# Kernel optimization log

Hardware: AMD Instinct MI355X
Metric: run time of the kernel (lower is better)

## Reference

```python
import jax, jax.numpy as jnp
import numpy as np

# static multi-scale pyramid (must match spatial_shapes array in setup_inputs)
SPATIAL = ((100, 100), (50, 50), (25, 25), (13, 13))
E, H, L, P = 256, 8, 4, 8   # embed_dims, num_heads, num_levels, num_points
BS, NQ = 2, 10000
LEN_VAL = sum(h * w for h, w in SPATIAL)


def _bilinear_gather(val, grid, Hs, Ws):
    """val: [BH, Hs*Ws, d]; grid: [BH, N, 2] in [-1,1].
    Matches F.grid_sample(mode='bilinear', padding_mode='zeros', align_corners=False)."""
    x = (grid[..., 0] + 1.0) * (Ws * 0.5) - 0.5
    y = (grid[..., 1] + 1.0) * (Hs * 0.5) - 0.5
    x0 = jnp.floor(x).astype(jnp.int32)
    y0 = jnp.floor(y).astype(jnp.int32)
    x1, y1 = x0 + 1, y0 + 1
    wx1 = x - x0.astype(x.dtype)
    wy1 = y - y0.astype(y.dtype)
    wx0, wy0 = 1.0 - wx1, 1.0 - wy1

    def corner(xi, yi, w):
        valid = (xi >= 0) & (xi < Ws) & (yi >= 0) & (yi < Hs)
        idx = jnp.clip(yi, 0, Hs - 1) * Ws + jnp.clip(xi, 0, Ws - 1)  # [BH, N]
        v = jnp.take_along_axis(val, idx[..., None], axis=1)          # [BH, N, d]
        return v * (w * valid.astype(w.dtype))[..., None]

    return (corner(x0, y0, wx0 * wy0) + corner(x1, y0, wx1 * wy0)
            + corner(x0, y1, wx0 * wy1) + corner(x1, y1, wx1 * wy1))


def setup_inputs() -> dict:
    key = jax.random.key(0)
    ks = jax.random.split(key, 10)
    scale = 1.0 / np.sqrt(E)
    inp = {
        'query': jax.random.normal(ks[0], (BS, NQ, E), jnp.float32),
        'value': jax.random.normal(ks[1], (BS, LEN_VAL, E), jnp.float32),
        'query_pos': 0.1 * jax.random.normal(ks[2], (BS, NQ, E), jnp.float32),
        'reference_points': jax.random.uniform(ks[3], (BS, NQ, L, 2), jnp.float32),
        'spatial_shapes': jnp.array(SPATIAL, dtype=jnp.int32),
        'W_off': 0.02 * jax.random.normal(ks[4], (E, H * L * P * 2), jnp.float32),
        'b_off': 0.5 * jax.random.normal(ks[5], (H * L * P * 2,), jnp.float32),
        'W_attn': 0.02 * jax.random.normal(ks[6], (E, H * L * P), jnp.float32),
        'b_attn': jnp.zeros((H * L * P,), jnp.float32),
        'W_val': scale * jax.random.normal(ks[7], (E, E), jnp.float32),
        'b_val': jnp.zeros((E,), jnp.float32),
        'W_out': scale * jax.random.normal(ks[8], (E, E), jnp.float32),
        'b_out': jnp.zeros((E,), jnp.float32),
    }
    return inp


def reference(query, value, query_pos, reference_points, spatial_shapes,
              W_off, b_off, W_attn, b_attn, W_val, b_val, W_out, b_out):
    d = E // H
    q = query + query_pos                                        # [bs, nq, E]
    bs, nq, _ = q.shape
    v = (value @ W_val + b_val).reshape(bs, LEN_VAL, H, d)       # [bs, len, H, d]
    off = (q @ W_off + b_off).reshape(bs, nq, H, L, P, 2)
    aw = jax.nn.softmax((q @ W_attn + b_attn).reshape(bs, nq, H, L * P), axis=-1)
    aw = aw.reshape(bs, nq, H, L, P)
    # normalizer is (W, H) per level
    norm = jnp.stack([spatial_shapes[:, 1], spatial_shapes[:, 0]], -1).astype(q.dtype)
    loc = reference_points[:, :, None, :, None, :] + off / norm[None, None, None, :, None, :]
    grids = 2.0 * loc - 1.0                                      # [bs, nq, H, L, P, 2]

    out = jnp.zeros((bs, nq, H, d), q.dtype)
    start = 0
    for lvl, (Hs, Ws) in enumerate(SPATIAL):
        v_l = v[:, start:start + Hs * Ws]                        # [bs, HW, H, d]
        start += Hs * Ws
        v_l = v_l.transpose(0, 2, 1, 3).reshape(bs * H, Hs * Ws, d)
        g_l = grids[:, :, :, lvl].transpose(0, 2, 1, 3, 4).reshape(bs * H, nq * P, 2)
        s = _bilinear_gather(v_l, g_l, Hs, Ws).reshape(bs, H, nq, P, d)
        w_l = aw[:, :, :, lvl].transpose(0, 2, 1, 3)             # [bs, H, nq, P]
        out = out + jnp.einsum('bhnpc,bhnp->bnhc', s, w_l)
    return out.reshape(bs, nq, E) @ W_out + b_out
```

## Files before the change

kernel.cpp:

```cpp
#include <hip/hip_runtime.h>


#define EE   256
#define HH   8
#define LL   4
#define NQq  10000
#define BSB  2
#define LENV 13294
#define MQ   16
#define ROWS_V (BSB * LENV)

#define VWS_OFF 393216

typedef unsigned short u16;
typedef unsigned int   u32;
typedef __attribute__((ext_vector_type(8))) short bf16x8;
typedef __attribute__((ext_vector_type(4))) float f32x4;

__device__ __forceinline__ u32 bf16_of(float f) {
  u32 u = __float_as_uint(f);
  return (u + 0x7FFFu + ((u >> 16) & 1u)) >> 16;
}
__device__ __forceinline__ float blo(u32 u) { return __uint_as_float(u << 16); }
__device__ __forceinline__ float bhi(u32 u) { return __uint_as_float(u & 0xFFFF0000u); }

__device__ __forceinline__ uint4 pack8(const float* f) {
  uint4 u;
  u.x = bf16_of(f[0]) | (bf16_of(f[1]) << 16);
  u.y = bf16_of(f[2]) | (bf16_of(f[3]) << 16);
  u.z = bf16_of(f[4]) | (bf16_of(f[5]) << 16);
  u.w = bf16_of(f[6]) | (bf16_of(f[7]) << 16);
  return u;
}

__device__ __forceinline__ void acc8(float o[8], uint4 q, float w) {
  o[0] += w * blo(q.x); o[1] += w * bhi(q.x);
  o[2] += w * blo(q.y); o[3] += w * bhi(q.y);
  o[4] += w * blo(q.z); o[5] += w * bhi(q.z);
  o[6] += w * blo(q.w); o[7] += w * bhi(q.w);
}

__global__ __launch_bounds__(64) void k_prep(
    const float* __restrict__ W_off, const float* __restrict__ W_attn,
    const float* __restrict__ W_val, const float* __restrict__ W_out,
    u16* __restrict__ wcat, u16* __restrict__ wval, u16* __restrict__ wout) {
  const int tile = blockIdx.x >> 3, s = blockIdx.x & 7;
  const int l = threadIdx.x, quad = l >> 4, r16 = l & 15;
  float f[8];
  u16* dst;
  if (tile < 48) {
    int col = tile * 16 + r16;
#pragma unroll
    for (int j = 0; j < 8; ++j) {
      int k = s * 32 + quad * 8 + j;
      f[j] = (col < 512) ? W_off[k * 512 + col] : W_attn[k * 256 + (col - 512)];
    }
    dst = wcat + ((tile * 8 + s) * 64 + l) * 8;
  } else if (tile < 64) {
    int col = (tile - 48) * 16 + r16;
#pragma unroll
    for (int j = 0; j < 8; ++j) f[j] = W_val[(s * 32 + quad * 8 + j) * 256 + col];
    dst = wval + (((tile - 48) * 8 + s) * 64 + l) * 8;
  } else {
    int col = (tile - 64) * 16 + r16;
#pragma unroll
    for (int j = 0; j < 8; ++j) f[j] = W_out[(s * 32 + quad * 8 + j) * 256 + col];
    dst = wout + (((tile - 64) * 8 + s) * 64 + l) * 8;
  }
  *(uint4*)dst = pack8(f);
}

__global__ __launch_bounds__(256) void k_valproj(
    const float* __restrict__ value, const float* __restrict__ b_val,
    const u16* __restrict__ wval, u16* __restrict__ v_ws) {
  __shared__ __align__(16) u16 sA[64][264];
  const int tid = threadIdx.x;
  const int g0 = blockIdx.x * 64;
#pragma unroll
  for (int ch = 0; ch < 8; ++ch) {
    int fidx = ch * 2048 + tid * 8;
    int row = fidx >> 8, col = fidx & 255;
    int g = g0 + row;
    float fv[8] = {0.f, 0.f, 0.f, 0.f, 0.f, 0.f, 0.f, 0.f};
    if (g < ROWS_V) {
      float4 a = *(const float4*)(value + (long)g * 256 + col);
      float4 b = *(const float4*)(value + (long)g * 256 + col + 4);
      fv[0] = a.x; fv[1] = a.y; fv[2] = a.z; fv[3] = a.w;
      fv[4] = b.x; fv[5] = b.y; fv[6] = b.z; fv[7] = b.w;
    }
    *(uint4*)&sA[row][col] = pack8(fv);
  }
  __syncthreads();
  const int wave = tid >> 6, lane = tid & 63, quad = lane >> 4, r16 = lane & 15;
  f32x4 acc[4][4] = {};
  for (int s = 0; s < 8; ++s) {
    bf16x8 af[4];
#pragma unroll
    for (int mt = 0; mt < 4; ++mt)
      af[mt] = *(const bf16x8*)&sA[mt * 16 + r16][s * 32 + quad * 8];
#pragma unroll
    for (int nt = 0; nt < 4; ++nt) {
      bf16x8 bfg = *(const bf16x8*)(wval + (((wave * 4 + nt) * 8 + s) * 64 + lane) * 8);
#pragma unroll
      for (int mt = 0; mt < 4; ++mt)
        acc[nt][mt] = __builtin_amdgcn_mfma_f32_16x16x32_bf16(af[mt], bfg, acc[nt][mt], 0, 0, 0);
    }
  }
  __syncthreads();
#pragma unroll
  for (int nt = 0; nt < 4; ++nt) {
    int col = (wave * 4 + nt) * 16 + r16;
    float bias = b_val[col];
#pragma unroll
    for (int mt = 0; mt < 4; ++mt)
#pragma unroll
      for (int rr = 0; rr < 4; ++rr)
        sA[mt * 16 + quad * 4 + rr][col] = (u16)bf16_of(acc[nt][mt][rr] + bias);
  }
  __syncthreads();
#pragma unroll
  for (int it = 0; it < 8; ++it) {
    int chunk = it * 256 + tid;
    int r  = chunk >> 5;
    int hc = chunk & 31;
    int h2 = hc >> 2, qq = hc & 3;
    int g = g0 + r;
    if (g < ROWS_V) {
      int bb = g / LENV, pix = g - bb * LENV;
      *(uint4*)(v_ws + ((long)((bb * 8 + h2) * LENV + pix) * 32 + qq * 8)) =
          *(const uint4*)&sA[r][h2 * 32 + qq * 8];
    }
  }
}

__global__ __launch_bounds__(512, 6) void k_attn(
    const float* __restrict__ query, const float* __restrict__ query_pos,
    const float* __restrict__ refpts,
    const float* __restrict__ b_off, const float* __restrict__ b_attn,
    const float* __restrict__ b_out,
    const u16* __restrict__ wcat, const u16* __restrict__ wout,
    const char* __restrict__ wsb, float* __restrict__ out) {
  __shared__ __align__(16) char smem[49408];
  u16   (*sQ)[264]   = (u16(*)[264])smem;
  float (*sC)[772]   = (float(*)[772])smem;
  uint2 (*sWgt)[256] = (uint2(*)[256])smem;
  u32   (*sOff)[256] = (u32(*)[256])(smem + 32768);
  u16   (*sO)[264]   = (u16(*)[264])smem;

  const int tid = threadIdx.x;
  const int g0 = blockIdx.x * MQ;
  const int b = g0 / NQq;
  const int q0 = g0 - b * NQq;
  const int wave = tid >> 6, lane = tid & 63, quad = lane >> 4, r16 = lane & 15;

  {
    int fidx = tid * 8;
    int row = fidx >> 8, col = fidx & 255;
    long base = ((long)(b * NQq + q0 + row)) * 256 + col;
    float4 a0 = *(const float4*)(query + base);
    float4 a1 = *(const float4*)(query + base + 4);
    float4 p0 = *(const float4*)(query_pos + base);
    float4 p1 = *(const float4*)(query_pos + base + 4);
    float fv[8] = {a0.x + p0.x, a0.y + p0.y, a0.z + p0.z, a0.w + p0.w,
                   a1.x + p1.x, a1.y + p1.y, a1.z + p1.z, a1.w + p1.w};
    *(uint4*)&sQ[row][col] = pack8(fv);
  }
  __syncthreads();

  f32x4 acc[6] = {};
  for (int s = 0; s < 8; ++s) {
    bf16x8 af = *(const bf16x8*)&sQ[r16][s * 32 + quad * 8];
#pragma unroll
    for (int t6 = 0; t6 < 6; ++t6) {
      int tile = wave * 6 + t6;
      bf16x8 bfg = *(const bf16x8*)(wcat + ((tile * 8 + s) * 64 + lane) * 8);
      acc[t6] = __builtin_amdgcn_mfma_f32_16x16x32_bf16(af, bfg, acc[t6], 0, 0, 0);
    }
  }
  __syncthreads();
#pragma unroll
  for (int t6 = 0; t6 < 6; ++t6) {
    int col = (wave * 6 + t6) * 16 + r16;
#pragma unroll
    for (int rr = 0; rr < 4; ++rr)
      sC[quad * 4 + rr][col] = acc[t6][rr];
  }
  __syncthreads();

  {
    const int m = tid >> 5, hh = (tid >> 2) & 7, g = tid & 3;
    float* p = &sC[m][512 + hh * 32 + g * 8];
    const float* ba = b_attn + hh * 32 + g * 8;
    float v[8];
    float mx = -1e30f;
#pragma unroll
    for (int j = 0; j < 8; ++j) { v[j] = p[j] + ba[j]; mx = fmaxf(mx, v[j]); }
    mx = fmaxf(mx, __shfl_xor(mx, 1));
    mx = fmaxf(mx, __shfl_xor(mx, 2));
    float sum = 0.f;
#pragma unroll
    for (int j = 0; j < 8; ++j) { v[j] = __expf(v[j] - mx); sum += v[j]; }
    sum += __shfl_xor(sum, 1);
    sum += __shfl_xor(sum, 2);
    float inv = 1.f / sum;
#pragma unroll
    for (int j = 0; j < 8; ++j) p[j] = v[j] * inv;
  }
  __syncthreads();

  uint2 wrecs[8];
  u32   orecs[8];
  {
    const int s = tid & 255, mh = tid >> 8;
    const int l = (s >> 3) & 3;
    const int WlI[4] = {100, 50, 25, 13};
    const int baseI[4] = {0, 10000, 12500, 13125};
    const int Wl = WlI[l], Hl = WlI[l], base = baseI[l];
    const float WlF = (float)Wl;
    const float box = b_off[2 * s], boy = b_off[2 * s + 1];
#pragma unroll
    for (int mm = 0; mm < 8; ++mm) {
      int m = mh * 8 + mm;
      float w = sC[m][512 + s];
      float ax = sC[m][2 * s], ay = sC[m][2 * s + 1];
      float2 rp = *(const float2*)(refpts + (((long)(b * NQq + q0 + m)) * LL + l) * 2);
      float x = rp.x * WlF + (ax + box) - 0.5f;
      float y = rp.y * WlF + (ay + boy) - 0.5f;
      float fx0 = floorf(x), fy0 = floorf(y);
      int x0 = (int)fx0, y0 = (int)fy0;
      float fx = x - fx0, fy = y - fy0;
      bool xv0 = (x0 >= 0) & (x0 < Wl);
      bool xv1 = (x0 >= -1) & (x0 < Wl - 1);
      bool yv0 = (y0 >= 0) & (y0 < Hl);
      bool yv1 = (y0 >= -1) & (y0 < Hl - 1);
      float w00 = w * (1.f - fx) * (1.f - fy) * (float)(xv0 & yv0);
      float w01 = w * fx * (1.f - fy) * (float)(xv1 & yv0);
      float w10 = w * (1.f - fx) * fy * (float)(xv0 & yv1);
      float w11 = w * fx * fy * (float)(xv1 & yv1);
      int x0a = min(max(x0, -1), Wl - 1);
      int y0a = min(max(y0, -1), Hl - 1);
      int y1c = min(max(y0 + 1, 0), Hl - 1);
      int o00u = base + y0a * Wl + x0a;
      u32 dyu  = (u32)((y1c - y0a) * Wl);
      wrecs[mm].x = bf16_of(w00) | (bf16_of(w01) << 16);
      wrecs[mm].y = bf16_of(w10) | (bf16_of(w11) << 16);
      orecs[mm]   = (u32)(o00u + 128) | (dyu << 14);
    }
  }
  __syncthreads();
  {
    const int s = tid & 255, mh = tid >> 8;
    const int jsw = (s & 224) | ((s + (s >> 5)) & 31);
#pragma unroll
    for (int mm = 0; mm < 8; ++mm) {
      sWgt[mh * 8 + mm][jsw] = wrecs[mm];
      sOff[mh * 8 + mm][jsw] = orecs[mm];
    }
  }
  __syncthreads();

  {
    const int c4 = tid & 3, hh = (tid >> 2) & 7, m = tid >> 5;
    const u32 vbm = (u32)VWS_OFF + (u32)(b * 8 + hh) * (u32)(LENV * 64)
                  + (u32)c4 * 16u - 8192u;
    float oacc[8] = {};
#pragma unroll 4
    for (int i = 0; i < 32; ++i) {
      const int srow = (hh << 5) | ((i + hh) & 31);
      uint2 wr = sWgt[m][srow];
      u32   po = sOff[m][srow];
      u32 off0 = vbm + ((po & 0x3FFFu) << 6);
      u32 off1 = off0 + ((po >> 14) << 6);
      uint4 q00 = *(const uint4*)(wsb + off0);
      uint4 q01 = *(const uint4*)(wsb + off0 + 64);
      uint4 q10 = *(const uint4*)(wsb + off1);
      uint4 q11 = *(const uint4*)(wsb + off1 + 64);
      float w00 = blo(wr.x), w01 = bhi(wr.x);
      float w10 = blo(wr.y), w11 = bhi(wr.y);
      acc8(oacc, q00, w00);
      acc8(oacc, q01, w01);
      acc8(oacc, q10, w10);
      acc8(oacc, q11, w11);
    }
    __syncthreads();
    *(uint4*)&sO[m][hh * 32 + c4 * 8] = pack8(oacc);
  }
  __syncthreads();

  f32x4 acc2[2] = {};
  for (int s = 0; s < 8; ++s) {
    bf16x8 af = *(const bf16x8*)&sO[r16][s * 32 + quad * 8];
#pragma unroll
    for (int t2 = 0; t2 < 2; ++t2) {
      int tile = wave * 2 + t2;
      bf16x8 bfg = *(const bf16x8*)(wout + ((tile * 8 + s) * 64 + lane) * 8);
      acc2[t2] = __builtin_amdgcn_mfma_f32_16x16x32_bf16(af, bfg, acc2[t2], 0, 0, 0);
    }
  }
#pragma unroll
  for (int t2 = 0; t2 < 2; ++t2) {
    int col = (wave * 2 + t2) * 16 + r16;
    float bias = b_out[col];
#pragma unroll
    for (int rr = 0; rr < 4; ++rr) {
      int row = quad * 4 + rr;
      out[((long)(b * NQq + q0 + row)) * 256 + col] = acc2[t2][rr] + bias;
    }
  }
}

extern "C" void kernel_launch(void* const* d_in, const int* in_sizes, int n_in,
                              void* d_out, int out_size, void* d_ws, size_t ws_size,
                              hipStream_t stream) {
  const float* query     = (const float*)d_in[0];
  const float* value     = (const float*)d_in[1];
  const float* query_pos = (const float*)d_in[2];
  const float* refpts    = (const float*)d_in[3];
  const float* W_off     = (const float*)d_in[5];
  const float* b_off     = (const float*)d_in[6];
  const float* W_attn    = (const float*)d_in[7];
  const float* b_attn    = (const float*)d_in[8];
  const float* W_val     = (const float*)d_in[9];
  const float* b_val     = (const float*)d_in[10];
  const float* W_out     = (const float*)d_in[11];
  const float* b_out     = (const float*)d_in[12];
  float* out = (float*)d_out;

  char* ws = (char*)d_ws;
  u16* wcat = (u16*)ws;
  u16* v_ws = (u16*)(ws + VWS_OFF);
  u16* wval = (u16*)(ws + VWS_OFF + 13613056);
  u16* wout = (u16*)(ws + VWS_OFF + 13613056 + 131072);

  k_prep<<<dim3(80 * 8), dim3(64), 0, stream>>>(W_off, W_attn, W_val, W_out,
                                                wcat, wval, wout);
  k_valproj<<<dim3((ROWS_V + 63) / 64), dim3(256), 0, stream>>>(value, b_val, wval, v_ws);
  k_attn<<<dim3(BSB * NQq / MQ), dim3(512), 0, stream>>>(
      query, query_pos, refpts, b_off, b_attn, b_out, wcat, wout, ws, out);
}
```

Measured before the change: 237.3 us.

## Fuse softmax into sampling setup, widen valproj blocks, unroll gather loop more

The value-projection kernel moves to 512 threads per block, with each wave computing two N-tiles instead of four, which lowers per-thread accumulator registers and gives more waves for latency hiding. The separate attention-weight softmax pass over shared memory, and its barrier, is removed. The softmax is now computed inside the sampling-record loop using 32-lane shuffle reductions over the 32 level×point logits per head. The gather loop unroll goes from 4 to 8 to expose more memory-level parallelism, at some register cost.

```diff
diff --git a/kernel.cpp b/kernel.cpp
--- a/kernel.cpp
+++ b/kernel.cpp
@@ -70,15 +70,15 @@
   *(uint4*)dst = pack8(f);
 }
 
-__global__ __launch_bounds__(256) void k_valproj(
+__global__ __launch_bounds__(512) void k_valproj(
     const float* __restrict__ value, const float* __restrict__ b_val,
     const u16* __restrict__ wval, u16* __restrict__ v_ws) {
   __shared__ __align__(16) u16 sA[64][264];
   const int tid = threadIdx.x;
   const int g0 = blockIdx.x * 64;
 #pragma unroll
-  for (int ch = 0; ch < 8; ++ch) {
-    int fidx = ch * 2048 + tid * 8;
+  for (int ch = 0; ch < 4; ++ch) {
+    int fidx = ch * 4096 + tid * 8;
     int row = fidx >> 8, col = fidx & 255;
     int g = g0 + row;
     float fv[8] = {0.f, 0.f, 0.f, 0.f, 0.f, 0.f, 0.f, 0.f};
@@ -92,15 +92,16 @@
   }
   __syncthreads();
   const int wave = tid >> 6, lane = tid & 63, quad = lane >> 4, r16 = lane & 15;
-  f32x4 acc[4][4] = {};
+  f32x4 acc[2][4] = {};
   for (int s = 0; s < 8; ++s) {
     bf16x8 af[4];
 #pragma unroll
     for (int mt = 0; mt < 4; ++mt)
       af[mt] = *(const bf16x8*)&sA[mt * 16 + r16][s * 32 + quad * 8];
 #pragma unroll
-    for (int nt = 0; nt < 4; ++nt) {
-      bf16x8 bfg = *(const bf16x8*)(wval + (((wave * 4 + nt) * 8 + s) * 64 + lane) * 8);
+    for (int nt = 0; nt < 2; ++nt) {
+      int ntg = wave * 2 + nt;
+      bf16x8 bfg = *(const bf16x8*)(wval + ((ntg * 8 + s) * 64 + lane) * 8);
 #pragma unroll
       for (int mt = 0; mt < 4; ++mt)
         acc[nt][mt] = __builtin_amdgcn_mfma_f32_16x16x32_bf16(af[mt], bfg, acc[nt][mt], 0, 0, 0);
@@ -108,8 +109,8 @@
   }
   __syncthreads();
 #pragma unroll
-  for (int nt = 0; nt < 4; ++nt) {
-    int col = (wave * 4 + nt) * 16 + r16;
+  for (int nt = 0; nt < 2; ++nt) {
+    int col = (wave * 2 + nt) * 16 + r16;
     float bias = b_val[col];
 #pragma unroll
     for (int mt = 0; mt < 4; ++mt)
@@ -119,8 +120,8 @@
   }
   __syncthreads();
 #pragma unroll
-  for (int it = 0; it < 8; ++it) {
-    int chunk = it * 256 + tid;
+  for (int it = 0; it < 4; ++it) {
+    int chunk = it * 512 + tid;
     int r  = chunk >> 5;
     int hc = chunk & 31;
     int h2 = hc >> 2, qq = hc & 3;
@@ -187,27 +188,6 @@
   }
   __syncthreads();
 
-  {
-    const int m = tid >> 5, hh = (tid >> 2) & 7, g = tid & 3;
-    float* p = &sC[m][512 + hh * 32 + g * 8];
-    const float* ba = b_attn + hh * 32 + g * 8;
-    float v[8];
-    float mx = -1e30f;
-#pragma unroll
-    for (int j = 0; j < 8; ++j) { v[j] = p[j] + ba[j]; mx = fmaxf(mx, v[j]); }
-    mx = fmaxf(mx, __shfl_xor(mx, 1));
-    mx = fmaxf(mx, __shfl_xor(mx, 2));
-    float sum = 0.f;
-#pragma unroll
-    for (int j = 0; j < 8; ++j) { v[j] = __expf(v[j] - mx); sum += v[j]; }
-    sum += __shfl_xor(sum, 1);
-    sum += __shfl_xor(sum, 2);
-    float inv = 1.f / sum;
-#pragma unroll
-    for (int j = 0; j < 8; ++j) p[j] = v[j] * inv;
-  }
-  __syncthreads();
-
   uint2 wrecs[8];
   u32   orecs[8];
   {
@@ -217,11 +197,26 @@
     const int baseI[4] = {0, 10000, 12500, 13125};
     const int Wl = WlI[l], Hl = WlI[l], base = baseI[l];
     const float WlF = (float)Wl;
+    const float ba  = b_attn[s];
     const float box = b_off[2 * s], boy = b_off[2 * s + 1];
 #pragma unroll
     for (int mm = 0; mm < 8; ++mm) {
       int m = mh * 8 + mm;
-      float w = sC[m][512 + s];
+      float logit = sC[m][512 + s] + ba;
+      float mx = logit;
+      mx = fmaxf(mx, __shfl_xor(mx, 1));
+      mx = fmaxf(mx, __shfl_xor(mx, 2));
+      mx = fmaxf(mx, __shfl_xor(mx, 4));
+      mx = fmaxf(mx, __shfl_xor(mx, 8));
+      mx = fmaxf(mx, __shfl_xor(mx, 16));
+      float e = __expf(logit - mx);
+      float sum = e;
+      sum += __shfl_xor(sum, 1);
+      sum += __shfl_xor(sum, 2);
+      sum += __shfl_xor(sum, 4);
+      sum += __shfl_xor(sum, 8);
+      sum += __shfl_xor(sum, 16);
+      float w = e * __frcp_rn(sum);
       float ax = sC[m][2 * s], ay = sC[m][2 * s + 1];
       float2 rp = *(const float2*)(refpts + (((long)(b * NQq + q0 + m)) * LL + l) * 2);
       float x = rp.x * WlF + (ax + box) - 0.5f;
@@ -264,7 +259,7 @@
     const u32 vbm = (u32)VWS_OFF + (u32)(b * 8 + hh) * (u32)(LENV * 64)
                   + (u32)c4 * 16u - 8192u;
     float oacc[8] = {};
-#pragma unroll 4
+#pragma unroll 8
     for (int i = 0; i < 32; ++i) {
       const int srow = (hh << 5) | ((i + hh) & 31);
       uint2 wr = sWgt[m][srow];
@@ -334,7 +329,7 @@
 
   k_prep<<<dim3(80 * 8), dim3(64), 0, stream>>>(W_off, W_attn, W_val, W_out,
                                                 wcat, wval, wout);
-  k_valproj<<<dim3((ROWS_V + 63) / 64), dim3(256), 0, stream>>>(value, b_val, wval, v_ws);
+  k_valproj<<<dim3((ROWS_V + 63) / 64), dim3(512), 0, stream>>>(value, b_val, wval, v_ws);
   k_attn<<<dim3(BSB * NQq / MQ), dim3(512), 0, stream>>>(
       query, query_pos, refpts, b_off, b_attn, b_out, wcat, wout, ws, out);
 }
```

Result: no change. 236.8 us (-0.2%).
